# Kernel tuning notes

Hardware: AMD Instinct MI355X
Metric: run time of the kernel (lower is better)

Reference implementation:

```python
import jax, jax.numpy as jnp
import numpy as np

N_NODES = 100000
N_EDGES = 1600000
IN_FEATS = 64
OUT_FEATS = 64
NEG_SLOPE = 0.2


def setup_inputs() -> dict:
    key = jax.random.key(0)
    ks = jax.random.split(key, 8)
    feat = jax.random.normal(ks[0], (N_NODES, IN_FEATS), dtype=jnp.float32)
    src = jax.random.randint(ks[1], (N_EDGES,), 0, N_NODES, dtype=jnp.int64 if jax.config.jax_enable_x64 else jnp.int32).astype(jnp.int32)
    dst = jax.random.randint(ks[2], (N_EDGES,), 0, N_NODES, dtype=jnp.int64 if jax.config.jax_enable_x64 else jnp.int32).astype(jnp.int32)
    scale = 1.0 / np.sqrt(IN_FEATS)
    Wq = jax.random.normal(ks[3], (IN_FEATS, OUT_FEATS), dtype=jnp.float32) * scale
    Wk = jax.random.normal(ks[4], (IN_FEATS, OUT_FEATS), dtype=jnp.float32) * scale
    Wf = jax.random.normal(ks[5], (IN_FEATS, OUT_FEATS), dtype=jnp.float32) * scale
    bq = jnp.zeros((OUT_FEATS,), dtype=jnp.float32)
    bk = jnp.zeros((OUT_FEATS,), dtype=jnp.float32)
    bf = jnp.zeros((OUT_FEATS,), dtype=jnp.float32)
    return {"feat": feat, "src": src, "dst": dst, "Wq": Wq, "bq": bq,
            "Wk": Wk, "bk": bk, "Wf": Wf, "bf": bf}


def reference(feat, src, dst, Wq, bq, Wk, bk, Wf, bf):
    N = feat.shape[0]
    # dense node projections (feat_drop=0 -> identity)
    q = feat @ Wq + bq          # [N, D] Query per destination node
    k = feat @ Wk + bk          # [N, D] Key per source node
    f = feat @ Wf + bf          # [N, D] message features
    # per-edge logit: u_dot_v(key, query)
    e = jnp.sum(k[src] * q[dst], axis=-1)              # [E]
    e = jax.nn.leaky_relu(e, negative_slope=NEG_SLOPE)
    # edge softmax grouped by destination node (numerically stable)
    emax = jax.ops.segment_max(e, dst, num_segments=N)  # [N]
    emax = jnp.where(jnp.isfinite(emax), emax, 0.0)     # empty segments -> 0
    ez = jnp.exp(e - emax[dst])                         # [E]
    denom = jax.ops.segment_sum(ez, dst, num_segments=N)  # [N]
    a = ez / denom[dst]                                  # [E] (attn_drop=0)
    # weighted scatter-sum aggregation: sum_e a_e * f[src_e] -> dst
    out = jax.ops.segment_sum(f[src] * a[:, None], dst, num_segments=N)  # [N, D]
    return out
```

## Files before the change

### kernel.cpp

```cpp
#include <hip/hip_runtime.h>
#include <math.h>

#define N_NODES   100000
#define N_EDGES   1600000
#define D         64
#define NEG_SLOPE 0.2f

#define SLOTS 56
#define ROW   64

#define NBUCK  256
#define BUCK_N 391
#define PK_SHIFT 9
#define PK_MASK  0x1FFu
#define CHUNK 2048
#define PART_BLOCKS ((N_EDGES + CHUNK - 1) / CHUNK)

typedef __attribute__((ext_vector_type(8))) _Float16 half8;
typedef __attribute__((ext_vector_type(2))) _Float16 half2v;
typedef __attribute__((ext_vector_type(4))) float floatx4;
typedef __attribute__((ext_vector_type(4))) int   intx4;

__device__ __forceinline__ unsigned short bfbits(float x) {
    unsigned u = __float_as_uint(x);
    u += 0x7fffu + ((u >> 16) & 1u);
    return (unsigned short)(u >> 16);
}
__device__ __forceinline__ float blo(unsigned v) { return __uint_as_float(v << 16); }
__device__ __forceinline__ float bhi(unsigned v) { return __uint_as_float(v & 0xffff0000u); }
__device__ __forceinline__ unsigned short h16(float x) {
    union { _Float16 h; unsigned short u; } c; c.h = (_Float16)x; return c.u;
}
__device__ __forceinline__ half2v u2h(unsigned v) {
    union { unsigned u; half2v h; } c; c.u = v; return c.h;
}
__device__ __forceinline__ float fdot2(unsigned a, half2v b, float c) {
#if __has_builtin(__builtin_amdgcn_fdot2)
    return __builtin_amdgcn_fdot2(u2h(a), b, c, false);
#else
    half2v ah = u2h(a);
    return c + (float)ah[0] * (float)b[0] + (float)ah[1] * (float)b[1];
#endif
}

#define WT_STRIDE 72
#define PROJ_BLOCKS 512
#define PROJ_WAVES  (PROJ_BLOCKS * 4)
#define FUSED_BLOCKS (PROJ_BLOCKS + PART_BLOCKS)

__global__ __launch_bounds__(256, 2) void proj_part_k(
    const float* __restrict__ feat,
    const float* __restrict__ Wq, const float* __restrict__ bq,
    const float* __restrict__ Wk, const float* __restrict__ bk,
    const float* __restrict__ Wf, const float* __restrict__ bf,
    unsigned short* __restrict__ qh, unsigned short* __restrict__ kf,
    const int* __restrict__ src, const int* __restrict__ dst,
    unsigned* __restrict__ pbuf, unsigned short* __restrict__ off16) {

    const int bx  = blockIdx.x;
    const int tid = threadIdx.x;

    __shared__ int smi[3 * 64 * WT_STRIDE / 2];

    if (bx >= PROJ_BLOCKS) {
        const int hid = bx - PROJ_BLOCKS;
        unsigned* ecache = (unsigned*)smi;
        int*      lcnt   = smi + CHUNK;
        int*      lsum   = smi + CHUNK + NBUCK;

        lcnt[tid] = 0;
        __syncthreads();

        int bkt[8]; int rnk[8]; unsigned pk[8];
        #pragma unroll
        for (int j = 0; j < 8; j++) bkt[j] = -1;

        const int cbase = hid * CHUNK;
        #pragma unroll
        for (int g = 0; g < 2; g++) {
            int eb = cbase + (g * 256 + tid) * 4;
            if (eb < N_EDGES) {
                intx4 d4 = __builtin_nontemporal_load((const intx4*)(dst + eb));
                intx4 s4 = __builtin_nontemporal_load((const intx4*)(src + eb));
                #pragma unroll
                for (int j = 0; j < 4; j++) {
                    int dd = (j == 0) ? d4.x : (j == 1) ? d4.y : (j == 2) ? d4.z : d4.w;
                    int ss = (j == 0) ? s4.x : (j == 1) ? s4.y : (j == 2) ? s4.z : s4.w;
                    int b  = dd / BUCK_N;
                    bkt[g * 4 + j] = b;
                    rnk[g * 4 + j] = atomicAdd(&lcnt[b], 1);
                    pk[g * 4 + j]  = ((unsigned)ss << PK_SHIFT)
                                   | (unsigned)(dd - b * BUCK_N);
                }
            }
        }
        __syncthreads();

        int own = lcnt[tid];
        lsum[tid] = own;
        __syncthreads();
        #pragma unroll
        for (int d2 = 1; d2 < NBUCK; d2 <<= 1) {
            int t = (tid >= d2) ? lsum[tid - d2] : 0;
            __syncthreads();
            lsum[tid] += t;
            __syncthreads();
        }
        int excl = lsum[tid] - own;

        off16[(size_t)hid * NBUCK + tid] = (unsigned short)excl;
        __syncthreads();
        lsum[tid] = excl;
        __syncthreads();

        #pragma unroll
        for (int j = 0; j < 8; j++) {
            int b = bkt[j];
            if (b >= 0) ecache[lsum[b] + rnk[j]] = pk[j];
        }
        __syncthreads();

        int total = N_EDGES - cbase; if (total > CHUNK) total = CHUNK;
        for (int i = tid; i < total; i += 256)
            pbuf[(size_t)hid * CHUNK + i] = ecache[i];
        return;
    }

    const int pid  = bx;
    unsigned short* wt = (unsigned short*)smi;

    const int lane = tid & 63;
    const int wave = tid >> 6;
    const int m    = lane & 15;
    const int quad = lane >> 4;

    for (int idx = tid; idx < 64 * 64; idx += 256) {
        int i = idx >> 6, dd = idx & 63;
        int o = dd * WT_STRIDE + i;
        wt[0 * 64 * WT_STRIDE + o] = h16(Wq[idx]);
        wt[1 * 64 * WT_STRIDE + o] = h16(Wk[idx]);
        wt[2 * 64 * WT_STRIDE + o] = h16(Wf[idx]);
    }
    __syncthreads();

    half8 Bf[3][4][2];
    float bias[3][4];
    #pragma unroll
    for (int w = 0; w < 3; w++)
        #pragma unroll
        for (int nt = 0; nt < 4; nt++) {
            int n = nt * 16 + m;
            #pragma unroll
            for (int ks = 0; ks < 2; ks++)
                Bf[w][nt][ks] = *(const half8*)&wt[(w * 64 + n) * WT_STRIDE + ks * 32 + quad * 8];
        }
    #pragma unroll
    for (int nt = 0; nt < 4; nt++) {
        int n = nt * 16 + m;
        bias[0][nt] = bq[n]; bias[1][nt] = bk[n]; bias[2][nt] = bf[n];
    }

    const int NT  = N_NODES / 16;
    const int wid = pid * 4 + wave;

    for (int t = wid; t < NT; t += PROJ_WAVES) {
        int t0  = t * 16;
        int row = t0 + m;

        const floatx4* fr = (const floatx4*)(feat + (size_t)row * D + quad * 8);
        floatx4 x0 = __builtin_nontemporal_load(fr);
        floatx4 x1 = __builtin_nontemporal_load(fr + 1);
        floatx4 x2 = __builtin_nontemporal_load(fr + 8);
        floatx4 x3 = __builtin_nontemporal_load(fr + 9);

        half8 a0, a1;
        a0[0] = (_Float16)x0.x; a0[1] = (_Float16)x0.y;
        a0[2] = (_Float16)x0.z; a0[3] = (_Float16)x0.w;
        a0[4] = (_Float16)x1.x; a0[5] = (_Float16)x1.y;
        a0[6] = (_Float16)x1.z; a0[7] = (_Float16)x1.w;
        a1[0] = (_Float16)x2.x; a1[1] = (_Float16)x2.y;
        a1[2] = (_Float16)x2.z; a1[3] = (_Float16)x2.w;
        a1[4] = (_Float16)x3.x; a1[5] = (_Float16)x3.y;
        a1[6] = (_Float16)x3.z; a1[7] = (_Float16)x3.w;

        floatx4 acc[3][4];
        #pragma unroll
        for (int w = 0; w < 3; w++)
            #pragma unroll
            for (int nt = 0; nt < 4; nt++) {
                floatx4 c = {bias[w][nt], bias[w][nt], bias[w][nt], bias[w][nt]};
                c = __builtin_amdgcn_mfma_f32_16x16x32_f16(a0, Bf[w][nt][0], c, 0, 0, 0);
                c = __builtin_amdgcn_mfma_f32_16x16x32_f16(a1, Bf[w][nt][1], c, 0, 0, 0);
                acc[w][nt] = c;
            }

        #pragma unroll
        for (int nt = 0; nt < 4; nt++) {
            int dim = nt * 16 + m;
            #pragma unroll
            for (int r = 0; r < 4; r++) {
                int node = t0 + quad * 4 + r;
                qh[(size_t)node * D + dim]        = h16(acc[0][nt][r]);
                kf[(size_t)node * 128 + dim]      = h16(acc[1][nt][r]);
                kf[(size_t)node * 128 + 64 + dim] = bfbits(acc[2][nt][r]);
            }
        }
    }
}

__global__ __launch_bounds__(1024) void build_k(
    const unsigned short* __restrict__ off16, const unsigned* __restrict__ pbuf,
    int* __restrict__ srcperm, int* __restrict__ counts) {

    const int b   = blockIdx.x;
    const int tid = threadIdx.x;

    __shared__ int cnt[BUCK_N];
    for (int i = tid; i < BUCK_N; i += 1024) cnt[i] = 0;
    __syncthreads();

    if (tid < PART_BLOCKS) {
        int o0 = off16[(size_t)tid * NBUCK + b];
        int o1;
        if (b < NBUCK - 1) {
            o1 = off16[(size_t)tid * NBUCK + b + 1];
        } else {
            o1 = N_EDGES - tid * CHUNK; if (o1 > CHUNK) o1 = CHUNK;
        }
        const unsigned* pp = pbuf + (size_t)tid * CHUNK;
        for (int r = o0; r < o1; r++) {
            unsigned p = pp[r];
            int loc = (int)(p & PK_MASK);
            int r2  = atomicAdd(&cnt[loc], 1);
            if (r2 < SLOTS)
                srcperm[(size_t)(b * BUCK_N + loc) * ROW + r2] =
                    (int)(p >> PK_SHIFT) << 8;
        }
    }
    __syncthreads();

    const int gbase = b * BUCK_N;
    for (int i = tid; i < BUCK_N; i += 1024) {
        int node = gbase + i;
        if (node < N_NODES) counts[node] = cnt[i];
    }
}

__global__ __launch_bounds__(256) void node_agg_k(
    const int* __restrict__ counts, const int* __restrict__ srcperm,
    const unsigned short* __restrict__ qh, const unsigned short* __restrict__ kf,
    float* __restrict__ out) {

    int wave = threadIdx.x >> 6;
    int lane = threadIdx.x & 63;
    int n    = blockIdx.x * 4 + wave;
    if (n >= N_NODES) return;

    const int l8 = lane & 7;
    const int eg = lane >> 3;

    int offs_all = srcperm[(size_t)n * ROW + lane];
    uint4 uq = *(const uint4*)(qh + (size_t)n * D + l8 * 8);
    half2v qp0 = u2h(uq.x), qp1 = u2h(uq.y), qp2 = u2h(uq.z), qp3 = u2h(uq.w);

    int deg = counts[n];
    if (deg > SLOTS) deg = SLOTS;

    const char* kfb = (const char*)kf;

    float acc[8] = {0, 0, 0, 0, 0, 0, 0, 0};
    float l = 0.0f;

    bool v   = eg < deg;
    int  off = __shfl(offs_all, eg);
    off = v ? off : 0;
    uint4 ku = *(const uint4*)(kfb + off + l8 * 16);
    uint4 fu = *(const uint4*)(kfb + off + 128 + l8 * 16);

    for (int i0 = 0; i0 < deg; i0 += 8) {
        bool hasnext = (i0 + 8) < deg;
        int  i2  = i0 + 8 + eg;
        bool v2  = i2 < deg;
        int  off2 = __shfl(offs_all, i2);
        off2 = v2 ? off2 : 0;
        uint4 kn = ku, fn = fu;
        if (hasnext) {
            kn = *(const uint4*)(kfb + off2 + l8 * 16);
            fn = *(const uint4*)(kfb + off2 + 128 + l8 * 16);
        }

        float dot = 0.0f;
        dot = fdot2(ku.x, qp0, dot);
        dot = fdot2(ku.y, qp1, dot);
        dot = fdot2(ku.z, qp2, dot);
        dot = fdot2(ku.w, qp3, dot);
        dot += __shfl_xor(dot, 1);
        dot += __shfl_xor(dot, 2);
        dot += __shfl_xor(dot, 4);

        float e  = dot > 0.0f ? dot : NEG_SLOPE * dot;
        e = fminf(e, 85.0f);
        float ez = v ? __expf(e) : 0.0f;
        l += ez;

        acc[0] = fmaf(ez, blo(fu.x), acc[0]);
        acc[1] = fmaf(ez, bhi(fu.x), acc[1]);
        acc[2] = fmaf(ez, blo(fu.y), acc[2]);
        acc[3] = fmaf(ez, bhi(fu.y), acc[3]);
        acc[4] = fmaf(ez, blo(fu.z), acc[4]);
        acc[5] = fmaf(ez, bhi(fu.z), acc[5]);
        acc[6] = fmaf(ez, blo(fu.w), acc[6]);
        acc[7] = fmaf(ez, bhi(fu.w), acc[7]);

        ku = kn; fu = fn; v = v2;
    }

    #pragma unroll
    for (int d2 = 8; d2 < 64; d2 <<= 1) {
        #pragma unroll
        for (int j = 0; j < 8; j++) acc[j] += __shfl_xor(acc[j], d2);
    }
    #pragma unroll
    for (int d2 = 1; d2 < 64; d2 <<= 1) l += __shfl_xor(l, d2);

    float inv = (deg > 0) ? 8.0f / fmaxf(l, 1e-30f) : 0.0f;
    if (eg == 0) {
        floatx4 o0 = {acc[0] * inv, acc[1] * inv, acc[2] * inv, acc[3] * inv};
        floatx4 o1 = {acc[4] * inv, acc[5] * inv, acc[6] * inv, acc[7] * inv};
        floatx4* op = (floatx4*)(out + (size_t)n * D + l8 * 8);
        __builtin_nontemporal_store(o0, op);
        __builtin_nontemporal_store(o1, op + 1);
    }
}

extern "C" void kernel_launch(void* const* d_in, const int* in_sizes, int n_in,
                              void* d_out, int out_size, void* d_ws, size_t ws_size,
                              hipStream_t stream) {
    const float* feat = (const float*)d_in[0];
    const int*   src  = (const int*)d_in[1];
    const int*   dst  = (const int*)d_in[2];
    const float* Wq   = (const float*)d_in[3];
    const float* bq   = (const float*)d_in[4];
    const float* Wk   = (const float*)d_in[5];
    const float* bk   = (const float*)d_in[6];
    const float* Wf   = (const float*)d_in[7];
    const float* bf   = (const float*)d_in[8];
    float* out = (float*)d_out;

    unsigned short* qh      = (unsigned short*)d_ws;
    unsigned short* kf      = qh + (size_t)N_NODES * D;
    int*            srcperm = (int*)(kf + (size_t)N_NODES * 2 * D);
    int*            counts  = srcperm + (size_t)N_NODES * ROW;

    unsigned*       pbuf  = (unsigned*)d_out;
    unsigned short* off16 = (unsigned short*)(pbuf + (size_t)PART_BLOCKS * CHUNK);

    proj_part_k<<<FUSED_BLOCKS, 256, 0, stream>>>(
        feat, Wq, bq, Wk, bk, Wf, bf, qh, kf, src, dst, pbuf, off16);

    build_k<<<NBUCK, 1024, 0, stream>>>(off16, pbuf, srcperm, counts);

    node_agg_k<<<(N_NODES + 3) / 4, 256, 0, stream>>>(counts, srcperm, qh, kf, out);
}
```

Before: 200.7 us.

## Fuse projection, partition and bucket build into one persistent kernel with grid barrier

Merges the projection/partition kernel and the bucket-build kernel into a single persistent kernel of 512 blocks. Each block first runs its share of edge partition chunks, signals an atomic arrival counter, does its projection work, then spins on the counter before 256 blocks do the bucket build. This is meant to remove a kernel launch boundary and to overlap the projection with the wait on other blocks' partition results. In exchange it adds a memset, a spin barrier that relies on all 512 blocks being co-resident, and a build phase that runs with 256 threads per block instead of 1024.

```diff
diff --git a/kernel.cpp b/kernel.cpp
--- a/kernel.cpp
+++ b/kernel.cpp
@@ -15,6 +15,8 @@
 #define PK_MASK  0x1FFu
 #define CHUNK 2048
 #define PART_BLOCKS ((N_EDGES + CHUNK - 1) / CHUNK)
+#define GRID 512
+#define NARRIVE GRID
 
 typedef __attribute__((ext_vector_type(8))) _Float16 half8;
 typedef __attribute__((ext_vector_type(2))) _Float16 half2v;
@@ -43,206 +45,223 @@
 #endif
 }
 
+__device__ __forceinline__ int bar_load(int* p) {
+#if __has_builtin(__hip_atomic_load)
+    return __hip_atomic_load(p, __ATOMIC_ACQUIRE, __HIP_MEMORY_SCOPE_AGENT);
+#else
+    return atomicAdd(p, 0);
+#endif
+}
+
 #define WT_STRIDE 72
-#define PROJ_BLOCKS 512
-#define PROJ_WAVES  (PROJ_BLOCKS * 4)
-#define FUSED_BLOCKS (PROJ_BLOCKS + PART_BLOCKS)
-
-__global__ __launch_bounds__(256, 2) void proj_part_k(
+#define PROJ_WAVES  (GRID * 4)
+
+__global__ __launch_bounds__(256, 2) void pre_k(
     const float* __restrict__ feat,
     const float* __restrict__ Wq, const float* __restrict__ bq,
     const float* __restrict__ Wk, const float* __restrict__ bk,
     const float* __restrict__ Wf, const float* __restrict__ bf,
     unsigned short* __restrict__ qh, unsigned short* __restrict__ kf,
     const int* __restrict__ src, const int* __restrict__ dst,
-    unsigned* __restrict__ pbuf, unsigned short* __restrict__ off16) {
+    unsigned* __restrict__ pbuf, unsigned short* __restrict__ off16,
+    int* __restrict__ srcperm, int* __restrict__ counts,
+    int* __restrict__ bar) {
 
     const int bx  = blockIdx.x;
     const int tid = threadIdx.x;
 
     __shared__ int smi[3 * 64 * WT_STRIDE / 2];
 
-    if (bx >= PROJ_BLOCKS) {
-        const int hid = bx - PROJ_BLOCKS;
+    {
         unsigned* ecache = (unsigned*)smi;
         int*      lcnt   = smi + CHUNK;
         int*      lsum   = smi + CHUNK + NBUCK;
 
-        lcnt[tid] = 0;
+        for (int hid = bx; hid < PART_BLOCKS; hid += GRID) {
+            lcnt[tid] = 0;
+            __syncthreads();
+
+            int bkt[8]; int rnk[8]; unsigned pk[8];
+            #pragma unroll
+            for (int j = 0; j < 8; j++) bkt[j] = -1;
+
+            const int cbase = hid * CHUNK;
+            #pragma unroll
+            for (int g = 0; g < 2; g++) {
+                int eb = cbase + (g * 256 + tid) * 4;
+                if (eb < N_EDGES) {
+                    intx4 d4 = __builtin_nontemporal_load((const intx4*)(dst + eb));
+                    intx4 s4 = __builtin_nontemporal_load((const intx4*)(src + eb));
+                    #pragma unroll
+                    for (int j = 0; j < 4; j++) {
+                        int dd = (j == 0) ? d4.x : (j == 1) ? d4.y : (j == 2) ? d4.z : d4.w;
+                        int ss = (j == 0) ? s4.x : (j == 1) ? s4.y : (j == 2) ? s4.z : s4.w;
+                        int b  = dd / BUCK_N;
+                        bkt[g * 4 + j] = b;
+                        rnk[g * 4 + j] = atomicAdd(&lcnt[b], 1);
+                        pk[g * 4 + j]  = ((unsigned)ss << PK_SHIFT)
+                                       | (unsigned)(dd - b * BUCK_N);
+                    }
+                }
+            }
+            __syncthreads();
+
+            int own = lcnt[tid];
+            lsum[tid] = own;
+            __syncthreads();
+            #pragma unroll
+            for (int d2 = 1; d2 < NBUCK; d2 <<= 1) {
+                int t = (tid >= d2) ? lsum[tid - d2] : 0;
+                __syncthreads();
+                lsum[tid] += t;
+                __syncthreads();
+            }
+            int excl = lsum[tid] - own;
+
+            off16[(size_t)hid * NBUCK + tid] = (unsigned short)excl;
+            __syncthreads();
+            lsum[tid] = excl;
+            __syncthreads();
+
+            #pragma unroll
+            for (int j = 0; j < 8; j++) {
+                int b = bkt[j];
+                if (b >= 0) ecache[lsum[b] + rnk[j]] = pk[j];
+            }
+            __syncthreads();
+
+            int total = N_EDGES - cbase; if (total > CHUNK) total = CHUNK;
+            for (int i = tid; i < total; i += 256)
+                pbuf[(size_t)hid * CHUNK + i] = ecache[i];
+        }
+    }
+
+    __syncthreads();
+    __threadfence();
+    if (tid == 0) atomicAdd(bar, 1);
+
+    {
         __syncthreads();
-
-        int bkt[8]; int rnk[8]; unsigned pk[8];
+        unsigned short* wt = (unsigned short*)smi;
+
+        const int lane = tid & 63;
+        const int wave = tid >> 6;
+        const int m    = lane & 15;
+        const int quad = lane >> 4;
+
+        for (int idx = tid; idx < 64 * 64; idx += 256) {
+            int i = idx >> 6, dd = idx & 63;
+            int o = dd * WT_STRIDE + i;
+            wt[0 * 64 * WT_STRIDE + o] = h16(Wq[idx]);
+            wt[1 * 64 * WT_STRIDE + o] = h16(Wk[idx]);
+            wt[2 * 64 * WT_STRIDE + o] = h16(Wf[idx]);
+        }
+        __syncthreads();
+
+        half8 Bf[3][4][2];
+        float bias[3][4];
         #pragma unroll
-        for (int j = 0; j < 8; j++) bkt[j] = -1;
-
-        const int cbase = hid * CHUNK;
-        #pragma unroll
-        for (int g = 0; g < 2; g++) {
-            int eb = cbase + (g * 256 + tid) * 4;
-            if (eb < N_EDGES) {
-                intx4 d4 = __builtin_nontemporal_load((const intx4*)(dst + eb));
-                intx4 s4 = __builtin_nontemporal_load((const intx4*)(src + eb));
+        for (int w = 0; w < 3; w++)
+            #pragma unroll
+            for (int nt = 0; nt < 4; nt++) {
+                int n = nt * 16 + m;
                 #pragma unroll
-                for (int j = 0; j < 4; j++) {
-                    int dd = (j == 0) ? d4.x : (j == 1) ? d4.y : (j == 2) ? d4.z : d4.w;
-                    int ss = (j == 0) ? s4.x : (j == 1) ? s4.y : (j == 2) ? s4.z : s4.w;
-                    int b  = dd / BUCK_N;
-                    bkt[g * 4 + j] = b;
-                    rnk[g * 4 + j] = atomicAdd(&lcnt[b], 1);
-                    pk[g * 4 + j]  = ((unsigned)ss << PK_SHIFT)
-                                   | (unsigned)(dd - b * BUCK_N);
-                }
-            }
-        }
-        __syncthreads();
-
-        int own = lcnt[tid];
-        lsum[tid] = own;
-        __syncthreads();
-        #pragma unroll
-        for (int d2 = 1; d2 < NBUCK; d2 <<= 1) {
-            int t = (tid >= d2) ? lsum[tid - d2] : 0;
-            __syncthreads();
-            lsum[tid] += t;
-            __syncthreads();
-        }
-        int excl = lsum[tid] - own;
-
-        off16[(size_t)hid * NBUCK + tid] = (unsigned short)excl;
-        __syncthreads();
-        lsum[tid] = excl;
-        __syncthreads();
-
-        #pragma unroll
-        for (int j = 0; j < 8; j++) {
-            int b = bkt[j];
-            if (b >= 0) ecache[lsum[b] + rnk[j]] = pk[j];
-        }
-        __syncthreads();
-
-        int total = N_EDGES - cbase; if (total > CHUNK) total = CHUNK;
-        for (int i = tid; i < total; i += 256)
-            pbuf[(size_t)hid * CHUNK + i] = ecache[i];
-        return;
-    }
-
-    const int pid  = bx;
-    unsigned short* wt = (unsigned short*)smi;
-
-    const int lane = tid & 63;
-    const int wave = tid >> 6;
-    const int m    = lane & 15;
-    const int quad = lane >> 4;
-
-    for (int idx = tid; idx < 64 * 64; idx += 256) {
-        int i = idx >> 6, dd = idx & 63;
-        int o = dd * WT_STRIDE + i;
-        wt[0 * 64 * WT_STRIDE + o] = h16(Wq[idx]);
-        wt[1 * 64 * WT_STRIDE + o] = h16(Wk[idx]);
-        wt[2 * 64 * WT_STRIDE + o] = h16(Wf[idx]);
-    }
-    __syncthreads();
-
-    half8 Bf[3][4][2];
-    float bias[3][4];
-    #pragma unroll
-    for (int w = 0; w < 3; w++)
+                for (int ks = 0; ks < 2; ks++)
+                    Bf[w][nt][ks] = *(const half8*)&wt[(w * 64 + n) * WT_STRIDE + ks * 32 + quad * 8];
+            }
         #pragma unroll
         for (int nt = 0; nt < 4; nt++) {
             int n = nt * 16 + m;
-            #pragma unroll
-            for (int ks = 0; ks < 2; ks++)
-                Bf[w][nt][ks] = *(const half8*)&wt[(w * 64 + n) * WT_STRIDE + ks * 32 + quad * 8];
-        }
-    #pragma unroll
-    for (int nt = 0; nt < 4; nt++) {
-        int n = nt * 16 + m;
-        bias[0][nt] = bq[n]; bias[1][nt] = bk[n]; bias[2][nt] = bf[n];
-    }
-
-    const int NT  = N_NODES / 16;
-    const int wid = pid * 4 + wave;
-
-    for (int t = wid; t < NT; t += PROJ_WAVES) {
-        int t0  = t * 16;
-        int row = t0 + m;
-
-        const floatx4* fr = (const floatx4*)(feat + (size_t)row * D + quad * 8);
-        floatx4 x0 = __builtin_nontemporal_load(fr);
-        floatx4 x1 = __builtin_nontemporal_load(fr + 1);
-        floatx4 x2 = __builtin_nontemporal_load(fr + 8);
-        floatx4 x3 = __builtin_nontemporal_load(fr + 9);
-
-        half8 a0, a1;
-        a0[0] = (_Float16)x0.x; a0[1] = (_Float16)x0.y;
-        a0[2] = (_Float16)x0.z; a0[3] = (_Float16)x0.w;
-        a0[4] = (_Float16)x1.x; a0[5] = (_Float16)x1.y;
-        a0[6] = (_Float16)x1.z; a0[7] = (_Float16)x1.w;
-        a1[0] = (_Float16)x2.x; a1[1] = (_Float16)x2.y;
-        a1[2] = (_Float16)x2.z; a1[3] = (_Float16)x2.w;
-        a1[4] = (_Float16)x3.x; a1[5] = (_Float16)x3.y;
-        a1[6] = (_Float16)x3.z; a1[7] = (_Float16)x3.w;
-
-        floatx4 acc[3][4];
-        #pragma unroll
-        for (int w = 0; w < 3; w++)
+            bias[0][nt] = bq[n]; bias[1][nt] = bk[n]; bias[2][nt] = bf[n];
+        }
+
+        const int NT  = N_NODES / 16;
+        const int wid = bx * 4 + wave;
+
+        for (int t = wid; t < NT; t += PROJ_WAVES) {
+            int t0  = t * 16;
+            int row = t0 + m;
+
+            const floatx4* fr = (const floatx4*)(feat + (size_t)row * D + quad * 8);
+            floatx4 x0 = __builtin_nontemporal_load(fr);
+            floatx4 x1 = __builtin_nontemporal_load(fr + 1);
+            floatx4 x2 = __builtin_nontemporal_load(fr + 8);
+            floatx4 x3 = __builtin_nontemporal_load(fr + 9);
+
+            half8 a0, a1;
+            a0[0] = (_Float16)x0.x; a0[1] = (_Float16)x0.y;
+            a0[2] = (_Float16)x0.z; a0[3] = (_Float16)x0.w;
+            a0[4] = (_Float16)x1.x; a0[5] = (_Float16)x1.y;
+            a0[6] = (_Float16)x1.z; a0[7] = (_Float16)x1.w;
+            a1[0] = (_Float16)x2.x; a1[1] = (_Float16)x2.y;
+            a1[2] = (_Float16)x2.z; a1[3] = (_Float16)x2.w;
+            a1[4] = (_Float16)x3.x; a1[5] = (_Float16)x3.y;
+            a1[6] = (_Float16)x3.z; a1[7] = (_Float16)x3.w;
+
+            floatx4 acc[3][4];
+            #pragma unroll
+            for (int w = 0; w < 3; w++)
+                #pragma unroll
+                for (int nt = 0; nt < 4; nt++) {
+                    floatx4 c = {bias[w][nt], bias[w][nt], bias[w][nt], bias[w][nt]};
+                    c = __builtin_amdgcn_mfma_f32_16x16x32_f16(a0, Bf[w][nt][0], c, 0, 0, 0);
+                    c = __builtin_amdgcn_mfma_f32_16x16x32_f16(a1, Bf[w][nt][1], c, 0, 0, 0);
+                    acc[w][nt] = c;
+                }
+
             #pragma unroll
             for (int nt = 0; nt < 4; nt++) {
-                floatx4 c = {bias[w][nt], bias[w][nt], bias[w][nt], bias[w][nt]};
-                c = __builtin_amdgcn_mfma_f32_16x16x32_f16(a0, Bf[w][nt][0], c, 0, 0, 0);
-                c = __builtin_amdgcn_mfma_f32_16x16x32_f16(a1, Bf[w][nt][1], c, 0, 0, 0);
-                acc[w][nt] = c;
-            }
-
-        #pragma unroll
-        for (int nt = 0; nt < 4; nt++) {
-            int dim = nt * 16 + m;
-            #pragma unroll
-            for (int r = 0; r < 4; r++) {
-                int node = t0 + quad * 4 + r;
-                qh[(size_t)node * D + dim]        = h16(acc[0][nt][r]);
-                kf[(size_t)node * 128 + dim]      = h16(acc[1][nt][r]);
-                kf[(size_t)node * 128 + 64 + dim] = bfbits(acc[2][nt][r]);
-            }
-        }
-    }
-}
-
-__global__ __launch_bounds__(1024) void build_k(
-    const unsigned short* __restrict__ off16, const unsigned* __restrict__ pbuf,
-    int* __restrict__ srcperm, int* __restrict__ counts) {
-
-    const int b   = blockIdx.x;
-    const int tid = threadIdx.x;
-
-    __shared__ int cnt[BUCK_N];
-    for (int i = tid; i < BUCK_N; i += 1024) cnt[i] = 0;
+                int dim = nt * 16 + m;
+                #pragma unroll
+                for (int r = 0; r < 4; r++) {
+                    int node = t0 + quad * 4 + r;
+                    qh[(size_t)node * D + dim]        = h16(acc[0][nt][r]);
+                    kf[(size_t)node * 128 + dim]      = h16(acc[1][nt][r]);
+                    kf[(size_t)node * 128 + 64 + dim] = bfbits(acc[2][nt][r]);
+                }
+            }
+        }
+    }
+
+    if (tid == 0) {
+        for (int s = 0; s < (1 << 21); ++s)
+            if (bar_load(bar) >= NARRIVE) break;
+    }
     __syncthreads();
-
-    if (tid < PART_BLOCKS) {
-        int o0 = off16[(size_t)tid * NBUCK + b];
-        int o1;
-        if (b < NBUCK - 1) {
-            o1 = off16[(size_t)tid * NBUCK + b + 1];
-        } else {
-            o1 = N_EDGES - tid * CHUNK; if (o1 > CHUNK) o1 = CHUNK;
-        }
-        const unsigned* pp = pbuf + (size_t)tid * CHUNK;
-        for (int r = o0; r < o1; r++) {
-            unsigned p = pp[r];
-            int loc = (int)(p & PK_MASK);
-            int r2  = atomicAdd(&cnt[loc], 1);
-            if (r2 < SLOTS)
-                srcperm[(size_t)(b * BUCK_N + loc) * ROW + r2] =
-                    (int)(p >> PK_SHIFT) << 8;
-        }
-    }
-    __syncthreads();
-
-    const int gbase = b * BUCK_N;
-    for (int i = tid; i < BUCK_N; i += 1024) {
-        int node = gbase + i;
-        if (node < N_NODES) counts[node] = cnt[i];
+    __threadfence();
+
+    if (bx >= NBUCK) return;
+    {
+        const int b = bx;
+        int* cnt = smi;
+        for (int i = tid; i < BUCK_N; i += 256) cnt[i] = 0;
+        __syncthreads();
+
+        for (int c = tid; c < PART_BLOCKS; c += 256) {
+            int o0 = off16[(size_t)c * NBUCK + b];
+            int o1;
+            if (b < NBUCK - 1) {
+                o1 = off16[(size_t)c * NBUCK + b + 1];
+            } else {
+                o1 = N_EDGES - c * CHUNK; if (o1 > CHUNK) o1 = CHUNK;
+            }
+            const unsigned* pp = pbuf + (size_t)c * CHUNK;
+            for (int r = o0; r < o1; r++) {
+                unsigned p = pp[r];
+                int loc = (int)(p & PK_MASK);
+                int r2  = atomicAdd(&cnt[loc], 1);
+                if (r2 < SLOTS)
+                    srcperm[(size_t)(b * BUCK_N + loc) * ROW + r2] =
+                        (int)(p >> PK_SHIFT) << 8;
+            }
+        }
+        __syncthreads();
+
+        const int gbase = b * BUCK_N;
+        for (int i = tid; i < BUCK_N; i += 256) {
+            int node = gbase + i;
+            if (node < N_NODES) counts[node] = cnt[i];
+        }
     }
 }
 
@@ -351,14 +370,16 @@
     unsigned short* kf      = qh + (size_t)N_NODES * D;
     int*            srcperm = (int*)(kf + (size_t)N_NODES * 2 * D);
     int*            counts  = srcperm + (size_t)N_NODES * ROW;
+    int*            bar     = counts + N_NODES;
 
     unsigned*       pbuf  = (unsigned*)d_out;
     unsigned short* off16 = (unsigned short*)(pbuf + (size_t)PART_BLOCKS * CHUNK);
 
-    proj_part_k<<<FUSED_BLOCKS, 256, 0, stream>>>(
-        feat, Wq, bq, Wk, bk, Wf, bf, qh, kf, src, dst, pbuf, off16);
-
-    build_k<<<NBUCK, 1024, 0, stream>>>(off16, pbuf, srcperm, counts);
+    hipMemsetAsync(bar, 0, sizeof(int), stream);
+
+    pre_k<<<GRID, 256, 0, stream>>>(
+        feat, Wq, bq, Wk, bk, Wf, bf, qh, kf, src, dst,
+        pbuf, off16, srcperm, counts, bar);
 
     node_agg_k<<<(N_NODES + 3) / 4, 256, 0, stream>>>(counts, srcperm, qh, kf, out);
 }
```

Measured after the change: 343.0 us. 70.9% more time.
